# Kernel tuning notes

Measured on AMD Instinct MI355X. Metric: run time of the kernel, lower is better.

## Reference

```python
import jax, jax.numpy as jnp
import numpy as np

EPS = 1e-6

def _log_g(x):
    # log of continuous g(x) = where(x>=0, x+0.5, sigmoid(x)) from minGRU paper
    return jnp.where(x >= 0, jnp.log(jax.nn.relu(x) + 0.5), -jax.nn.softplus(-x))

def setup_inputs() -> dict:
    key = jax.random.key(0)
    ks = jax.random.split(key, 4)
    B, S, D, E = 4, 2048, 1024, 8
    scale = D ** -0.5
    return {
        "inputs": jax.random.normal(ks[0], (B, S, D), dtype=jnp.float32),
        "norm_weight": jnp.ones((D,), jnp.float32),
        "router_w": jax.random.normal(ks[1], (E, D), jnp.float32) * scale,
        "router_b": jnp.zeros((E,), jnp.float32),
        "w_hg": jax.random.normal(ks[2], (E, 2 * D, D), jnp.float32) * scale,
        "w_out": jax.random.normal(ks[3], (E, D, D), jnp.float32) * scale,
    }

def reference(inputs, norm_weight, router_w, router_b, w_hg, w_out):
    D = inputs.shape[-1]
    # --- RMSNorm ---
    x = inputs * jax.lax.rsqrt(jnp.mean(inputs * inputs, axis=-1, keepdims=True) + EPS) * norm_weight
    # --- SMEAR: per-sample soft merge of expert weights via mean-pooled routing ---
    probs = jax.nn.softmax(jnp.mean(x, axis=1) @ router_w.T + router_b, axis=-1)  # [B,E]
    W_hg = jnp.einsum('be,ekd->bkd', probs, w_hg)    # [B,2D,D] merged to_hidden_and_gate
    W_out = jnp.einsum('be,eod->bod', probs, w_out)  # [B,D,D]  merged to_out
    # --- minGRU with merged weights (log-space parallel scan, no initial state) ---
    hg = jnp.einsum('bsd,bkd->bsk', x, W_hg)         # [B,S,2D]
    hidden, gate = hg[..., :D], hg[..., D:]
    log_coeffs = -jax.nn.softplus(gate)                      # log(1 - z_t)
    log_values = -jax.nn.softplus(-gate) + _log_g(hidden)    # log z_t + log g(h~_t)
    a_star = jnp.cumsum(log_coeffs, axis=1)
    log_h = a_star + jax.lax.cumlogsumexp(log_values - a_star, axis=1)
    h = jnp.exp(log_h)                               # [B,S,D] recurrent states
    new_state = h[:, -1:]                            # [B,1,D]
    out = jnp.einsum('bsk,bok->bso', h, W_out)       # proj_out
    aux_loss = jnp.zeros((), inputs.dtype)
    return (out + inputs, new_state, aux_loss)
```

## Files before the change

### kernel.cpp

```cpp
#include <hip/hip_runtime.h>
#include <hip/hip_bf16.h>
#include <hip/hip_fp16.h>

#define B_  4
#define S_  2048
#define D_  1024
#define E_  8
#define K2_ 2048

#define CHUNKS 64
#define CLEN   32

typedef __attribute__((ext_vector_type(8))) short short8;
typedef __attribute__((ext_vector_type(4))) float floatx4;

__device__ __forceinline__ void gld16(const void* g, const void* l) {
    __builtin_amdgcn_global_load_lds(
        (const __attribute__((address_space(1))) unsigned int*)g,
        (__attribute__((address_space(3))) unsigned int*)l, 16, 0, 0);
}

__device__ __forceinline__ unsigned short f2bf(float f) {
    unsigned int u = __float_as_uint(f);
    u += 0x7fffu + ((u >> 16) & 1u);
    return (unsigned short)(u >> 16);
}

__global__ void rmsnorm_k(const float* __restrict__ in, const float* __restrict__ nw,
                          __hip_bfloat16* __restrict__ x) {
    int b = blockIdx.y, s = blockIdx.x, t = threadIdx.x;
    const float4* row = (const float4*)(in + ((size_t)b * S_ + s) * D_);
    float4 v = row[t];
    float ss = v.x * v.x + v.y * v.y + v.z * v.z + v.w * v.w;
#pragma unroll
    for (int o = 32; o > 0; o >>= 1) ss += __shfl_down(ss, o, 64);
    __shared__ float ls[4];
    if ((t & 63) == 0) ls[t >> 6] = ss;
    __syncthreads();
    float tot = ls[0] + ls[1] + ls[2] + ls[3];
    float rs = rsqrtf(tot * (1.0f / (float)D_) + 1e-6f);
    float4 w = ((const float4*)nw)[t];
    ushort4 o;
    o.x = f2bf(v.x * rs * w.x); o.y = f2bf(v.y * rs * w.y);
    o.z = f2bf(v.z * rs * w.z); o.w = f2bf(v.w * rs * w.w);
    ((ushort4*)(x + ((size_t)b * S_ + s) * D_))[t] = o;
}

__global__ void xsum_k(const __hip_bfloat16* __restrict__ x, float* __restrict__ xs) {
    int d = blockIdx.x * 256 + threadIdx.x;
    int b = blockIdx.y;
    int s0 = blockIdx.z * 128;
    const __hip_bfloat16* p = x + ((size_t)b * S_ + s0) * D_ + d;
    float acc = 0.0f;
#pragma unroll 4
    for (int s = 0; s < 128; s++) { acc += __bfloat162float(*p); p += D_; }
    atomicAdd(&xs[b * D_ + d], acc);
}

__global__ void router_k(const float* __restrict__ xs, const float* __restrict__ rw,
                         const float* __restrict__ rb, float* __restrict__ probs,
                         float* __restrict__ aux) {
    int t = threadIdx.x;
    if (t == 255) *aux = 0.0f;
    int pair = t >> 3, sub = t & 7;
    int b = pair >> 3, e = pair & 7;
    float acc = 0.0f;
#pragma unroll 8
    for (int d = sub; d < D_; d += 8) acc += xs[b * D_ + d] * rw[e * D_ + d];
#pragma unroll
    for (int o = 4; o > 0; o >>= 1) acc += __shfl_down(acc, o, 8);
    __shared__ float lg[32];
    if (sub == 0) lg[pair] = acc * (1.0f / (float)S_) + rb[e];
    __syncthreads();
    if (t < 4) {
        float m = -1e30f;
        for (int e2 = 0; e2 < 8; e2++) m = fmaxf(m, lg[t * 8 + e2]);
        float ssum = 0.0f; float ex[8];
        for (int e2 = 0; e2 < 8; e2++) { ex[e2] = expf(lg[t * 8 + e2] - m); ssum += ex[e2]; }
        for (int e2 = 0; e2 < 8; e2++) probs[t * 8 + e2] = ex[e2] / ssum;
    }
}

__global__ void mix_k(const float* __restrict__ probs, const float* __restrict__ whg_e,
                      const float* __restrict__ wout_e, __hip_bfloat16* __restrict__ Whg,
                      __hip_bfloat16* __restrict__ Wout) {
    __shared__ float P[32];
    int t = threadIdx.x;
    if (t < 32) P[t] = probs[t];
    __syncthreads();
    size_t i4 = (size_t)blockIdx.x * 256 + t;
    const size_t T1q = (size_t)K2_ * D_ / 4;
    const size_t T2q = (size_t)D_ * D_ / 4;
    float4 a0 = {0,0,0,0}, a1 = {0,0,0,0}, a2 = {0,0,0,0}, a3 = {0,0,0,0};
    if (i4 < T1q) {
        const float4* src = (const float4*)whg_e;
#pragma unroll
        for (int e = 0; e < 8; e++) {
            float4 wv = src[(size_t)e * T1q + i4];
            float p0 = P[e], p1 = P[8 + e], p2 = P[16 + e], p3 = P[24 + e];
            a0.x += p0 * wv.x; a0.y += p0 * wv.y; a0.z += p0 * wv.z; a0.w += p0 * wv.w;
            a1.x += p1 * wv.x; a1.y += p1 * wv.y; a1.z += p1 * wv.z; a1.w += p1 * wv.w;
            a2.x += p2 * wv.x; a2.y += p2 * wv.y; a2.z += p2 * wv.z; a2.w += p2 * wv.w;
            a3.x += p3 * wv.x; a3.y += p3 * wv.y; a3.z += p3 * wv.z; a3.w += p3 * wv.w;
        }
        ushort4* dst = (ushort4*)Whg;
        ushort4 o;
        o.x = f2bf(a0.x); o.y = f2bf(a0.y); o.z = f2bf(a0.z); o.w = f2bf(a0.w);
        dst[0 * T1q + i4] = o;
        o.x = f2bf(a1.x); o.y = f2bf(a1.y); o.z = f2bf(a1.z); o.w = f2bf(a1.w);
        dst[1 * T1q + i4] = o;
        o.x = f2bf(a2.x); o.y = f2bf(a2.y); o.z = f2bf(a2.z); o.w = f2bf(a2.w);
        dst[2 * T1q + i4] = o;
        o.x = f2bf(a3.x); o.y = f2bf(a3.y); o.z = f2bf(a3.z); o.w = f2bf(a3.w);
        dst[3 * T1q + i4] = o;
    } else {
        size_t j4 = i4 - T1q;
        const float4* src = (const float4*)wout_e;
#pragma unroll
        for (int e = 0; e < 8; e++) {
            float4 wv = src[(size_t)e * T2q + j4];
            float p0 = P[e], p1 = P[8 + e], p2 = P[16 + e], p3 = P[24 + e];
            a0.x += p0 * wv.x; a0.y += p0 * wv.y; a0.z += p0 * wv.z; a0.w += p0 * wv.w;
            a1.x += p1 * wv.x; a1.y += p1 * wv.y; a1.z += p1 * wv.z; a1.w += p1 * wv.w;
            a2.x += p2 * wv.x; a2.y += p2 * wv.y; a2.z += p2 * wv.z; a2.w += p2 * wv.w;
            a3.x += p3 * wv.x; a3.y += p3 * wv.y; a3.z += p3 * wv.z; a3.w += p3 * wv.w;
        }
        ushort4* dst = (ushort4*)Wout;
        ushort4 o;
        o.x = f2bf(a0.x); o.y = f2bf(a0.y); o.z = f2bf(a0.z); o.w = f2bf(a0.w);
        dst[0 * T2q + j4] = o;
        o.x = f2bf(a1.x); o.y = f2bf(a1.y); o.z = f2bf(a1.z); o.w = f2bf(a1.w);
        dst[1 * T2q + j4] = o;
        o.x = f2bf(a2.x); o.y = f2bf(a2.y); o.z = f2bf(a2.z); o.w = f2bf(a2.w);
        dst[2 * T2q + j4] = o;
        o.x = f2bf(a3.x); o.y = f2bf(a3.y); o.z = f2bf(a3.z); o.w = f2bf(a3.w);
        dst[3 * T2q + j4] = o;
    }
}

__global__ __launch_bounds__(256) void gemm_hg_cv(
    const __hip_bfloat16* __restrict__ A, const __hip_bfloat16* __restrict__ Bm,
    __half2* __restrict__ cv) {
    const int K = D_;
    int bz = blockIdx.z;
    A  += (size_t)bz * S_ * D_;
    Bm += (size_t)bz * K2_ * D_;
    __half2* CV = cv + (size_t)bz * S_ * D_;
    int m0 = blockIdx.y * 128, n0 = blockIdx.x * 64;
    __shared__ __hip_bfloat16 lA[2][128][64];
    __shared__ __hip_bfloat16 lBh[2][64][64];
    __shared__ __hip_bfloat16 lBg[2][64][64];
    int t = threadIdx.x;
    int w = t >> 6, lane = t & 63;
    int lm = lane & 15, quad = lane >> 4;
    int wr = w >> 1, wc = w & 1;
    floatx4 acch[4][2] = {};
    floatx4 accg[4][2] = {};
    int srow = lane >> 3;
    int swzb = ((lane & 7) ^ srow) * 16;

    const __hip_bfloat16* Bh = Bm;
    const __hip_bfloat16* Bg = Bm + (size_t)D_ * K;

    auto stage = [&](int bb, int k0) {
#pragma unroll
        for (int it = 0; it < 4; it++) {
            int r0 = (w * 4 + it) * 8;
            gld16((const char*)(A + (size_t)(m0 + r0 + srow) * K + k0) + swzb,
                  &lA[bb][r0][0]);
        }
#pragma unroll
        for (int it = 0; it < 2; it++) {
            int r0 = (w * 2 + it) * 8;
            gld16((const char*)(Bh + (size_t)(n0 + r0 + srow) * K + k0) + swzb,
                  &lBh[bb][r0][0]);
            gld16((const char*)(Bg + (size_t)(n0 + r0 + srow) * K + k0) + swzb,
                  &lBg[bb][r0][0]);
        }
    };

    stage(0, 0);
    int cur = 0;
    for (int k0 = 0; k0 < K; k0 += 64) {
        if (k0 + 64 < K) {
            stage(cur ^ 1, k0 + 64);
            asm volatile("s_waitcnt vmcnt(8)" ::: "memory");
        } else {
            asm volatile("s_waitcnt vmcnt(0)" ::: "memory");
        }
        __builtin_amdgcn_s_barrier();
#pragma unroll
        for (int kk = 0; kk < 64; kk += 32) {
            short8 af[4], bh[2], bg[2];
            int p = (((kk >> 3) + quad) ^ (lm & 7)) * 8;
#pragma unroll
            for (int i = 0; i < 4; i++)
                af[i] = *(const short8*)(&lA[cur][wr * 64 + i * 16 + lm][p]);
#pragma unroll
            for (int j = 0; j < 2; j++) {
                bh[j] = *(const short8*)(&lBh[cur][wc * 32 + j * 16 + lm][p]);
                bg[j] = *(const short8*)(&lBg[cur][wc * 32 + j * 16 + lm][p]);
            }
#pragma unroll
            for (int i = 0; i < 4; i++)
#pragma unroll
                for (int j = 0; j < 2; j++) {
                    acch[i][j] = __builtin_amdgcn_mfma_f32_16x16x32_bf16(
                        af[i], bh[j], acch[i][j], 0, 0, 0);
                    accg[i][j] = __builtin_amdgcn_mfma_f32_16x16x32_bf16(
                        af[i], bg[j], accg[i][j], 0, 0, 0);
                }
        }
        asm volatile("s_waitcnt lgkmcnt(0)" ::: "memory");
        __builtin_amdgcn_s_barrier();
        cur ^= 1;
    }
#pragma unroll
    for (int i = 0; i < 4; i++) {
#pragma unroll
        for (int j = 0; j < 2; j++) {
#pragma unroll
            for (int r = 0; r < 4; r++) {
                int m = m0 + wr * 64 + i * 16 + quad * 4 + r;
                int n = n0 + wc * 32 + j * 16 + lm;
                float hid = acch[i][j][r];
                float g   = accg[i][j][r];
                float eg  = expf(g);
                float c   = 1.0f / (1.0f + eg);
                float sg  = 1.0f - c;
                float gfn = (hid >= 0.0f) ? (hid + 0.5f)
                                          : (1.0f / (1.0f + expf(-hid)));
                CV[(size_t)m * D_ + n] = __floats2half2_rn(c, sg * gfn);
            }
        }
    }
}

#define TM 128
#define TN 128
#define TBK 64
__global__ __launch_bounds__(256) void gemm_bf16_bt(
    const __hip_bfloat16* __restrict__ A, const __hip_bfloat16* __restrict__ Bm,
    float* __restrict__ C, const float* __restrict__ R,
    int M, int N, int K, size_t sa, size_t sb, size_t sc, size_t sr) {
    int bz = blockIdx.z;
    A += (size_t)bz * sa; Bm += (size_t)bz * sb; C += (size_t)bz * sc;
    if (R) R += (size_t)bz * sr;
    int m0 = blockIdx.y * TM, n0 = blockIdx.x * TN;
    __shared__ __hip_bfloat16 lA[2][TM][TBK];
    __shared__ __hip_bfloat16 lB[2][TN][TBK];
    int t = threadIdx.x;
    int w = t >> 6, lane = t & 63;
    int lm = lane & 15, quad = lane >> 4;
    int wr = w >> 1, wc = w & 1;
    floatx4 acc[4][4] = {};
    int srow = lane >> 3;
    int swzb = ((lane & 7) ^ srow) * 16;

    auto stage = [&](int bb, int k0) {
#pragma unroll
        for (int it = 0; it < 4; it++) {
            int r0 = (w * 4 + it) * 8;
            gld16((const char*)(A + (size_t)(m0 + r0 + srow) * K + k0) + swzb,
                  &lA[bb][r0][0]);
            gld16((const char*)(Bm + (size_t)(n0 + r0 + srow) * K + k0) + swzb,
                  &lB[bb][r0][0]);
        }
    };

    stage(0, 0);
    int cur = 0;
    for (int k0 = 0; k0 < K; k0 += TBK) {
        if (k0 + TBK < K) {
            stage(cur ^ 1, k0 + TBK);
            asm volatile("s_waitcnt vmcnt(8)" ::: "memory");
        } else {
            asm volatile("s_waitcnt vmcnt(0)" ::: "memory");
        }
        __builtin_amdgcn_s_barrier();
#pragma unroll
        for (int kk = 0; kk < TBK; kk += 32) {
            short8 af[4], bf[4];
            int p = (((kk >> 3) + quad) ^ (lm & 7)) * 8;
#pragma unroll
            for (int i = 0; i < 4; i++)
                af[i] = *(const short8*)(&lA[cur][wr * 64 + i * 16 + lm][p]);
#pragma unroll
            for (int j = 0; j < 4; j++)
                bf[j] = *(const short8*)(&lB[cur][wc * 64 + j * 16 + lm][p]);
#pragma unroll
            for (int i = 0; i < 4; i++)
#pragma unroll
                for (int j = 0; j < 4; j++)
                    acc[i][j] = __builtin_amdgcn_mfma_f32_16x16x32_bf16(
                        af[i], bf[j], acc[i][j], 0, 0, 0);
        }
        asm volatile("s_waitcnt lgkmcnt(0)" ::: "memory");
        __builtin_amdgcn_s_barrier();
        cur ^= 1;
    }
#pragma unroll
    for (int i = 0; i < 4; i++) {
#pragma unroll
        for (int j = 0; j < 4; j++) {
#pragma unroll
            for (int r = 0; r < 4; r++) {
                int m = m0 + wr * 64 + i * 16 + quad * 4 + r;
                int n = n0 + wc * 64 + j * 16 + lm;
                float v = acc[i][j][r];
                if (R) v += R[(size_t)m * N + n];
                C[(size_t)m * N + n] = v;
            }
        }
    }
}

__global__ void scanA_k(const __half2* __restrict__ cv, float* __restrict__ Cc,
                        float* __restrict__ Vc) {
    int c = blockIdx.x, b = blockIdx.y, t = threadIdx.x;
    const float4* p = (const float4*)(cv + (size_t)(b * S_ + c * CLEN) * D_) + t;
    float P0 = 1, P1 = 1, P2 = 1, P3 = 1;
    float V0 = 0, V1 = 0, V2 = 0, V3 = 0;
#pragma unroll 4
    for (int s = 0; s < CLEN; s++) {
        float4 raw = p[(size_t)s * (D_ / 4)];
        const __half2* e = (const __half2*)&raw;
        float c0 = __low2float(e[0]), v0 = __high2float(e[0]);
        float c1 = __low2float(e[1]), v1 = __high2float(e[1]);
        float c2 = __low2float(e[2]), v2 = __high2float(e[2]);
        float c3 = __low2float(e[3]), v3 = __high2float(e[3]);
        P0 *= c0; V0 = fmaf(c0, V0, v0);
        P1 *= c1; V1 = fmaf(c1, V1, v1);
        P2 *= c2; V2 = fmaf(c2, V2, v2);
        P3 *= c3; V3 = fmaf(c3, V3, v3);
    }
    size_t q = ((size_t)(b * CHUNKS + c)) * (D_ / 4) + t;
    ((float4*)Cc)[q] = make_float4(P0, P1, P2, P3);
    ((float4*)Vc)[q] = make_float4(V0, V1, V2, V3);
}

__global__ void scanC_k(const __half2* __restrict__ cv, const float* __restrict__ Cc,
                        const float* __restrict__ Vc,
                        __hip_bfloat16* __restrict__ hout, float* __restrict__ ns) {
    int c = blockIdx.x, b = blockIdx.y, t = threadIdx.x;
    float h0 = 0, h1 = 0, h2 = 0, h3 = 0;
#pragma unroll 4
    for (int cc = 0; cc < c; cc++) {
        size_t q = ((size_t)(b * CHUNKS + cc)) * (D_ / 4) + t;
        float4 C4 = ((const float4*)Cc)[q];
        float4 V4 = ((const float4*)Vc)[q];
        h0 = fmaf(C4.x, h0, V4.x); h1 = fmaf(C4.y, h1, V4.y);
        h2 = fmaf(C4.z, h2, V4.z); h3 = fmaf(C4.w, h3, V4.w);
    }
    const float4* p = (const float4*)(cv + (size_t)(b * S_ + c * CLEN) * D_) + t;
    ushort4* hq = (ushort4*)(hout + (size_t)(b * S_ + c * CLEN) * D_) + t;
#pragma unroll 4
    for (int s = 0; s < CLEN; s++) {
        float4 raw = p[(size_t)s * (D_ / 4)];
        const __half2* e = (const __half2*)&raw;
        h0 = fmaf(__low2float(e[0]), h0, __high2float(e[0]));
        h1 = fmaf(__low2float(e[1]), h1, __high2float(e[1]));
        h2 = fmaf(__low2float(e[2]), h2, __high2float(e[2]));
        h3 = fmaf(__low2float(e[3]), h3, __high2float(e[3]));
        ushort4 o;
        o.x = f2bf(h0); o.y = f2bf(h1); o.z = f2bf(h2); o.w = f2bf(h3);
        hq[(size_t)s * (D_ / 4)] = o;
    }
    if (c == CHUNKS - 1)
        ((float4*)(ns + (size_t)b * D_))[t] = make_float4(h0, h1, h2, h3);
}

extern "C" void kernel_launch(void* const* d_in, const int* in_sizes, int n_in,
                              void* d_out_v, int out_size, void* d_ws, size_t ws_size,
                              hipStream_t stream) {
    const float* inputs = (const float*)d_in[0];
    const float* nw     = (const float*)d_in[1];
    const float* rw     = (const float*)d_in[2];
    const float* rb     = (const float*)d_in[3];
    const float* whg_e  = (const float*)d_in[4];
    const float* wout_e = (const float*)d_in[5];
    float* out = (float*)d_out_v;

    float* ws = (float*)d_ws;
    __half2*        cv      = (__half2*)ws;
    __hip_bfloat16* x_bf    = (__hip_bfloat16*)(ws + 8388608);
    __hip_bfloat16* h_bf    = (__hip_bfloat16*)(ws + 12582912);
    __hip_bfloat16* Whg_bf  = (__hip_bfloat16*)(ws + 16777216);
    __hip_bfloat16* Wout_bf = (__hip_bfloat16*)(ws + 20971520);
    float* xsum  = ws + 23068672;
    float* probs = ws + 23072768;
    float* Cc    = ws + 23072800;
    float* Vc    = ws + 23334944;

    hipMemsetAsync(xsum, 0, (size_t)B_ * D_ * sizeof(float), stream);

    rmsnorm_k<<<dim3(S_, B_), 256, 0, stream>>>(inputs, nw, x_bf);
    xsum_k<<<dim3(D_ / 256, B_, 16), 256, 0, stream>>>(x_bf, xsum);
    router_k<<<1, 256, 0, stream>>>(xsum, rw, rb, probs,
                                    out + (size_t)B_ * S_ * D_ + (size_t)B_ * D_);
    mix_k<<<3072, 256, 0, stream>>>(probs, whg_e, wout_e, Whg_bf, Wout_bf);

    gemm_hg_cv<<<dim3(D_ / 64, S_ / 128, B_), 256, 0, stream>>>(x_bf, Whg_bf, cv);

    scanA_k<<<dim3(CHUNKS, B_), 256, 0, stream>>>(cv, Cc, Vc);
    scanC_k<<<dim3(CHUNKS, B_), 256, 0, stream>>>(
        cv, Cc, Vc, h_bf, out + (size_t)B_ * S_ * D_);

    gemm_bf16_bt<<<dim3(D_ / TN, S_ / TM, B_), 256, 0, stream>>>(
        h_bf, Wout_bf, out, inputs, S_, D_, D_,
        (size_t)S_ * D_, (size_t)D_ * D_, (size_t)S_ * D_, (size_t)S_ * D_);
}
```

Baseline: 309.5 us.

## Restructure GEMM main loops: one barrier per tile, incremental pointers, MFMA priority

Result: no change. 311.8 us (+0.7%).

```diff
diff --git a/kernel.cpp b/kernel.cpp
--- a/kernel.cpp
+++ b/kernel.cpp
@@ -158,61 +158,83 @@
     floatx4 accg[4][2] = {};
     int srow = lane >> 3;
     int swzb = ((lane & 7) ^ srow) * 16;
+    int pb = (quad ^ (lm & 7)) * 16;
 
     const __hip_bfloat16* Bh = Bm;
     const __hip_bfloat16* Bg = Bm + (size_t)D_ * K;
 
-    auto stage = [&](int bb, int k0) {
+    const char* pA[4]; const char* pBhp[2]; const char* pBgp[2];
+#pragma unroll
+    for (int it = 0; it < 4; it++)
+        pA[it] = (const char*)(A + (size_t)(m0 + (w * 4 + it) * 8 + srow) * K) + swzb;
+#pragma unroll
+    for (int it = 0; it < 2; it++) {
+        pBhp[it] = (const char*)(Bh + (size_t)(n0 + (w * 2 + it) * 8 + srow) * K) + swzb;
+        pBgp[it] = (const char*)(Bg + (size_t)(n0 + (w * 2 + it) * 8 + srow) * K) + swzb;
+    }
+
+    auto stage = [&](int bb) {
 #pragma unroll
         for (int it = 0; it < 4; it++) {
-            int r0 = (w * 4 + it) * 8;
-            gld16((const char*)(A + (size_t)(m0 + r0 + srow) * K + k0) + swzb,
-                  &lA[bb][r0][0]);
+            gld16(pA[it], &lA[bb][(w * 4 + it) * 8][0]);
+            pA[it] += 128;
         }
 #pragma unroll
         for (int it = 0; it < 2; it++) {
-            int r0 = (w * 2 + it) * 8;
-            gld16((const char*)(Bh + (size_t)(n0 + r0 + srow) * K + k0) + swzb,
-                  &lBh[bb][r0][0]);
-            gld16((const char*)(Bg + (size_t)(n0 + r0 + srow) * K + k0) + swzb,
-                  &lBg[bb][r0][0]);
+            gld16(pBhp[it], &lBh[bb][(w * 2 + it) * 8][0]); pBhp[it] += 128;
+            gld16(pBgp[it], &lBg[bb][(w * 2 + it) * 8][0]); pBgp[it] += 128;
         }
     };
 
-    stage(0, 0);
+    stage(0);
+    asm volatile("s_waitcnt vmcnt(0)" ::: "memory");
+    __builtin_amdgcn_s_barrier();
     int cur = 0;
     for (int k0 = 0; k0 < K; k0 += 64) {
-        if (k0 + 64 < K) {
-            stage(cur ^ 1, k0 + 64);
-            asm volatile("s_waitcnt vmcnt(8)" ::: "memory");
-        } else {
+        bool pre = (k0 + 64 < K);
+        short8 af0[4], bh0[2], bg0[2];
+#pragma unroll
+        for (int i = 0; i < 4; i++)
+            af0[i] = *(const short8*)((const char*)&lA[cur][wr * 64 + i * 16 + lm][0] + pb);
+#pragma unroll
+        for (int j = 0; j < 2; j++) {
+            bh0[j] = *(const short8*)((const char*)&lBh[cur][wc * 32 + j * 16 + lm][0] + pb);
+            bg0[j] = *(const short8*)((const char*)&lBg[cur][wc * 32 + j * 16 + lm][0] + pb);
+        }
+        if (pre) stage(cur ^ 1);
+        __builtin_amdgcn_s_setprio(1);
+#pragma unroll
+        for (int i = 0; i < 4; i++)
+#pragma unroll
+            for (int j = 0; j < 2; j++) {
+                acch[i][j] = __builtin_amdgcn_mfma_f32_16x16x32_bf16(
+                    af0[i], bh0[j], acch[i][j], 0, 0, 0);
+                accg[i][j] = __builtin_amdgcn_mfma_f32_16x16x32_bf16(
+                    af0[i], bg0[j], accg[i][j], 0, 0, 0);
+            }
+        short8 af1[4], bh1[2], bg1[2];
+#pragma unroll
+        for (int i = 0; i < 4; i++)
+            af1[i] = *(const short8*)((const char*)&lA[cur][wr * 64 + i * 16 + lm][0] + (pb ^ 64));
+#pragma unroll
+        for (int j = 0; j < 2; j++) {
+            bh1[j] = *(const short8*)((const char*)&lBh[cur][wc * 32 + j * 16 + lm][0] + (pb ^ 64));
+            bg1[j] = *(const short8*)((const char*)&lBg[cur][wc * 32 + j * 16 + lm][0] + (pb ^ 64));
+        }
+#pragma unroll
+        for (int i = 0; i < 4; i++)
+#pragma unroll
+            for (int j = 0; j < 2; j++) {
+                acch[i][j] = __builtin_amdgcn_mfma_f32_16x16x32_bf16(
+                    af1[i], bh1[j], acch[i][j], 0, 0, 0);
+                accg[i][j] = __builtin_amdgcn_mfma_f32_16x16x32_bf16(
+                    af1[i], bg1[j], accg[i][j], 0, 0, 0);
+            }
+        __builtin_amdgcn_s_setprio(0);
+        if (pre) {
             asm volatile("s_waitcnt vmcnt(0)" ::: "memory");
-        }
-        __builtin_amdgcn_s_barrier();
-#pragma unroll
-        for (int kk = 0; kk < 64; kk += 32) {
-            short8 af[4], bh[2], bg[2];
-            int p = (((kk >> 3) + quad) ^ (lm & 7)) * 8;
-#pragma unroll
-            for (int i = 0; i < 4; i++)
-                af[i] = *(const short8*)(&lA[cur][wr * 64 + i * 16 + lm][p]);
-#pragma unroll
-            for (int j = 0; j < 2; j++) {
-                bh[j] = *(const short8*)(&lBh[cur][wc * 32 + j * 16 + lm][p]);
-                bg[j] = *(const short8*)(&lBg[cur][wc * 32 + j * 16 + lm][p]);
-            }
-#pragma unroll
-            for (int i = 0; i < 4; i++)
-#pragma unroll
-                for (int j = 0; j < 2; j++) {
-                    acch[i][j] = __builtin_amdgcn_mfma_f32_16x16x32_bf16(
-                        af[i], bh[j], acch[i][j], 0, 0, 0);
-                    accg[i][j] = __builtin_amdgcn_mfma_f32_16x16x32_bf16(
-                        af[i], bg[j], accg[i][j], 0, 0, 0);
-                }
-        }
-        asm volatile("s_waitcnt lgkmcnt(0)" ::: "memory");
-        __builtin_amdgcn_s_barrier();
+            __builtin_amdgcn_s_barrier();
+        }
         cur ^= 1;
     }
 #pragma unroll
@@ -256,47 +278,62 @@
     floatx4 acc[4][4] = {};
     int srow = lane >> 3;
     int swzb = ((lane & 7) ^ srow) * 16;
-
-    auto stage = [&](int bb, int k0) {
+    int pb = (quad ^ (lm & 7)) * 16;
+
+    const char* pA[4]; const char* pB[4];
+#pragma unroll
+    for (int it = 0; it < 4; it++) {
+        pA[it] = (const char*)(A + (size_t)(m0 + (w * 4 + it) * 8 + srow) * K) + swzb;
+        pB[it] = (const char*)(Bm + (size_t)(n0 + (w * 4 + it) * 8 + srow) * K) + swzb;
+    }
+
+    auto stage = [&](int bb) {
 #pragma unroll
         for (int it = 0; it < 4; it++) {
-            int r0 = (w * 4 + it) * 8;
-            gld16((const char*)(A + (size_t)(m0 + r0 + srow) * K + k0) + swzb,
-                  &lA[bb][r0][0]);
-            gld16((const char*)(Bm + (size_t)(n0 + r0 + srow) * K + k0) + swzb,
-                  &lB[bb][r0][0]);
+            gld16(pA[it], &lA[bb][(w * 4 + it) * 8][0]); pA[it] += 128;
+            gld16(pB[it], &lB[bb][(w * 4 + it) * 8][0]); pB[it] += 128;
         }
     };
 
-    stage(0, 0);
+    stage(0);
+    asm volatile("s_waitcnt vmcnt(0)" ::: "memory");
+    __builtin_amdgcn_s_barrier();
     int cur = 0;
     for (int k0 = 0; k0 < K; k0 += TBK) {
-        if (k0 + TBK < K) {
-            stage(cur ^ 1, k0 + TBK);
-            asm volatile("s_waitcnt vmcnt(8)" ::: "memory");
-        } else {
+        bool pre = (k0 + TBK < K);
+        short8 af0[4], bf0[4];
+#pragma unroll
+        for (int i = 0; i < 4; i++)
+            af0[i] = *(const short8*)((const char*)&lA[cur][wr * 64 + i * 16 + lm][0] + pb);
+#pragma unroll
+        for (int j = 0; j < 4; j++)
+            bf0[j] = *(const short8*)((const char*)&lB[cur][wc * 64 + j * 16 + lm][0] + pb);
+        if (pre) stage(cur ^ 1);
+        __builtin_amdgcn_s_setprio(1);
+#pragma unroll
+        for (int i = 0; i < 4; i++)
+#pragma unroll
+            for (int j = 0; j < 4; j++)
+                acc[i][j] = __builtin_amdgcn_mfma_f32_16x16x32_bf16(
+                    af0[i], bf0[j], acc[i][j], 0, 0, 0);
+        short8 af1[4], bf1[4];
+#pragma unroll
+        for (int i = 0; i < 4; i++)
+            af1[i] = *(const short8*)((const char*)&lA[cur][wr * 64 + i * 16 + lm][0] + (pb ^ 64));
+#pragma unroll
+        for (int j = 0; j < 4; j++)
+            bf1[j] = *(const short8*)((const char*)&lB[cur][wc * 64 + j * 16 + lm][0] + (pb ^ 64));
+#pragma unroll
+        for (int i = 0; i < 4; i++)
+#pragma unroll
+            for (int j = 0; j < 4; j++)
+                acc[i][j] = __builtin_amdgcn_mfma_f32_16x16x32_bf16(
+                    af1[i], bf1[j], acc[i][j], 0, 0, 0);
+        __builtin_amdgcn_s_setprio(0);
+        if (pre) {
             asm volatile("s_waitcnt vmcnt(0)" ::: "memory");
-        }
-        __builtin_amdgcn_s_barrier();
-#pragma unroll
-        for (int kk = 0; kk < TBK; kk += 32) {
-            short8 af[4], bf[4];
-            int p = (((kk >> 3) + quad) ^ (lm & 7)) * 8;
-#pragma unroll
-            for (int i = 0; i < 4; i++)
-                af[i] = *(const short8*)(&lA[cur][wr * 64 + i * 16 + lm][p]);
-#pragma unroll
-            for (int j = 0; j < 4; j++)
-                bf[j] = *(const short8*)(&lB[cur][wc * 64 + j * 16 + lm][p]);
-#pragma unroll
-            for (int i = 0; i < 4; i++)
-#pragma unroll
-                for (int j = 0; j < 4; j++)
-                    acc[i][j] = __builtin_amdgcn_mfma_f32_16x16x32_bf16(
-                        af[i], bf[j], acc[i][j], 0, 0, 0);
-        }
-        asm volatile("s_waitcnt lgkmcnt(0)" ::: "memory");
-        __builtin_amdgcn_s_barrier();
+            __builtin_amdgcn_s_barrier();
+        }
         cur ^= 1;
     }
 #pragma unroll
```
